# Kernel tuning notes

Hardware: AMD Instinct MI355X
Metric: run time of the kernel (lower is better)

The kernel has to match this reference:

```python
import jax, jax.numpy as jnp
import numpy as np

B, L, D, N, V = 32, 4096, 128, 5, 128  # batch, seq, embed dim, n-gram order, alphabet size


def setup_inputs() -> dict:
    key = jax.random.key(0)
    k1, k2, k3 = jax.random.split(key, 3)
    x = jax.random.randint(k1, (B, L), 0, V, dtype=jnp.int32)
    emb = jax.random.normal(k2, (V, D), dtype=jnp.float32)
    W = jax.random.normal(k3, (V, D * (N - 1)), dtype=jnp.float32) * 0.05
    b = jnp.zeros((V,), dtype=jnp.float32)
    return {"x": x, "emb": emb, "W": W, "b": b}


def reference(x, emb, W, b):
    n1 = N - 1  # context window size
    x_enc = emb[x]  # (B, L, D) embedding gather
    # enc[:, j, k*D:(k+1)*D] = x_enc[:, j - n1 + k] for j >= n1; zeros for j < n1.
    # Build each slot by right-shifting the embedded sequence by (n1 - k).
    Lcur = x.shape[1]
    parts = [jnp.pad(x_enc, ((0, 0), (n1 - k, 0), (0, 0)))[:, :Lcur] for k in range(n1)]
    enc = jnp.concatenate(parts, axis=-1)  # (B, L, n1*D)
    valid = (jnp.arange(Lcur) >= n1)[None, :, None]
    enc = jnp.where(valid, enc, jnp.zeros((), enc.dtype))
    # linear: logits = enc @ W^T + b  -> (B, L, V)
    logits = jnp.einsum("blf,vf->blv", enc, W) + b
    return logits
```

## Files before the change

kernel.cpp:

```cpp
#include <hip/hip_runtime.h>

constexpr int Bn = 32;
constexpr int Ln = 4096;
constexpr int Dn = 128;
constexpr int Vn = 128;
constexpr int N1 = 4;

typedef float vfloat4 __attribute__((ext_vector_type(4)));

__global__ void build_table_kernel(const float* __restrict__ emb,
                                   const float* __restrict__ W,
                                   const float* __restrict__ bias,
                                   float* __restrict__ T) {
    const int kt = blockIdx.x;
    const int k  = kt >> 7;
    const int t  = kt & 127;
    const int v  = threadIdx.x;

    __shared__ float4 e[Dn / 4];
    if (threadIdx.x < Dn / 4) {
        e[threadIdx.x] = ((const float4*)(emb + t * Dn))[threadIdx.x];
    }
    __syncthreads();

    const float4* w = (const float4*)(W + (size_t)v * (Dn * N1) + k * Dn);
    float acc = (k == 0) ? bias[v] : 0.f;
#pragma unroll
    for (int i = 0; i < Dn / 4; ++i) {
        float4 wv = w[i];
        float4 ev = e[i];
        acc += wv.x * ev.x + wv.y * ev.y + wv.z * ev.z + wv.w * ev.w;
    }
    T[(size_t)kt * Vn + v] = acc;
}

__global__ void __launch_bounds__(256)
ngram_logits_kernel(const int* __restrict__ x,
                    const float* __restrict__ T,
                    const float* __restrict__ bias,
                    float* __restrict__ out) {
    const int tid     = blockIdx.x * blockDim.x + threadIdx.x;
    const int vq      = tid & 31;
    const int g       = tid >> 5;
    const int basepos = g << 2;
    const int j0      = basepos & (Ln - 1);

    vfloat4* outq = (vfloat4*)out;

    if (j0 == 0) {
        const vfloat4 bv = ((const vfloat4*)bias)[vq];
#pragma unroll
        for (int i = 0; i < 4; ++i)
            __builtin_nontemporal_store(bv, &outq[(size_t)(basepos + i) * 32 + vq]);
        return;
    }

    const int4 xa = *(const int4*)(x + basepos - 4);
    const int4 xb = *(const int4*)(x + basepos);
    int w[7] = {xa.x, xa.y, xa.z, xa.w, xb.x, xb.y, xb.z};

    const vfloat4* Tq = (const vfloat4*)T;
    vfloat4 acc[4];
#pragma unroll
    for (int i = 0; i < 4; ++i) {
        vfloat4 a = Tq[(size_t)(0 * Vn + w[i + 0]) * 32 + vq];
#pragma unroll
        for (int k = 1; k < N1; ++k) {
            a += Tq[(size_t)(k * Vn + w[i + k]) * 32 + vq];
        }
        acc[i] = a;
    }

#pragma unroll
    for (int i = 0; i < 4; ++i)
        __builtin_nontemporal_store(acc[i], &outq[(size_t)(basepos + i) * 32 + vq]);
}

extern "C" void kernel_launch(void* const* d_in, const int* in_sizes, int n_in,
                              void* d_out, int out_size, void* d_ws, size_t ws_size,
                              hipStream_t stream) {
    const int*   x    = (const int*)d_in[0];
    const float* emb  = (const float*)d_in[1];
    const float* W    = (const float*)d_in[2];
    const float* bias = (const float*)d_in[3];
    float*       out  = (float*)d_out;
    float*       T    = (float*)d_ws;

    build_table_kernel<<<N1 * Vn, Vn, 0, stream>>>(emb, W, bias, T);

    const int total_threads = (Bn * Ln / 4) * (Vn / 4);
    const int block = 256;
    ngram_logits_kernel<<<total_threads / block, block, 0, stream>>>(x, T, bias, out);
}
```

Baseline: 92.77 us.

## Stage vocab-sliced n-gram table in LDS and gather from shared memory

The precomputed table is re-laid out into 8 vocab slices of 16 columns each. Each block copies its 32 KB slice into padded LDS (row stride 20 floats to reduce bank conflicts) and then serves 1024 positions for that slice from LDS rather than from global or L2. Each block covers only 16 output columns, so every output row is written as 64-byte chunks, and the x indices are read once for each of the 8 slices. The launch moves to 1024 blocks of 512 threads.

```diff
diff --git a/kernel.cpp b/kernel.cpp
--- a/kernel.cpp
+++ b/kernel.cpp
@@ -31,49 +31,66 @@
         float4 ev = e[i];
         acc += wv.x * ev.x + wv.y * ev.y + wv.z * ev.z + wv.w * ev.w;
     }
-    T[(size_t)kt * Vn + v] = acc;
+    T[(size_t)(((v >> 4) * N1 + k) * Vn + t) * 16 + (v & 15)] = acc;
 }
 
-__global__ void __launch_bounds__(256)
+constexpr int ROWS    = N1 * Vn;
+constexpr int RSTRIDE = 20;
+
+__global__ void __launch_bounds__(512, 8)
 ngram_logits_kernel(const int* __restrict__ x,
                     const float* __restrict__ T,
                     const float* __restrict__ bias,
                     float* __restrict__ out) {
-    const int tid     = blockIdx.x * blockDim.x + threadIdx.x;
-    const int vq      = tid & 31;
-    const int g       = tid >> 5;
-    const int basepos = g << 2;
-    const int j0      = basepos & (Ln - 1);
+    __shared__ float lds[ROWS * RSTRIDE];
 
-    vfloat4* outq = (vfloat4*)out;
+    const int e  = blockIdx.x & 7;
+    const int pb = blockIdx.x >> 3;
 
-    if (j0 == 0) {
-        const vfloat4 bv = ((const vfloat4*)bias)[vq];
+    {
+        const float4* src = (const float4*)(T + (size_t)e * (ROWS * 16));
+        float4*       dst = (float4*)lds;
 #pragma unroll
-        for (int i = 0; i < 4; ++i)
-            __builtin_nontemporal_store(bv, &outq[(size_t)(basepos + i) * 32 + vq]);
-        return;
+        for (int it = 0; it < 4; ++it) {
+            const int f = it * 512 + threadIdx.x;
+            const int r = f >> 2;
+            const int c = f & 3;
+            dst[r * (RSTRIDE / 4) + c] = src[f];
+        }
     }
+    __syncthreads();
 
-    const int4 xa = *(const int4*)(x + basepos - 4);
-    const int4 xb = *(const int4*)(x + basepos);
-    int w[7] = {xa.x, xa.y, xa.z, xa.w, xb.x, xb.y, xb.z};
-
-    const vfloat4* Tq = (const vfloat4*)T;
-    vfloat4 acc[4];
-#pragma unroll
-    for (int i = 0; i < 4; ++i) {
-        vfloat4 a = Tq[(size_t)(0 * Vn + w[i + 0]) * 32 + vq];
-#pragma unroll
-        for (int k = 1; k < N1; ++k) {
-            a += Tq[(size_t)(k * Vn + w[i + k]) * 32 + vq];
-        }
-        acc[i] = a;
-    }
+    const int vq = threadIdx.x & 3;
+    const int gl = threadIdx.x >> 2;
+    const vfloat4* lv   = (const vfloat4*)lds;
+    vfloat4*       outq = (vfloat4*)out;
 
 #pragma unroll
-    for (int i = 0; i < 4; ++i)
-        __builtin_nontemporal_store(acc[i], &outq[(size_t)(basepos + i) * 32 + vq]);
+    for (int it = 0; it < 2; ++it) {
+        const int basepos = pb * 1024 + it * 512 + gl * 4;
+        vfloat4*  ob      = outq + (size_t)basepos * 32 + e * 4 + vq;
+
+        if ((basepos & (Ln - 1)) == 0) {
+            const vfloat4 bv = ((const vfloat4*)bias)[e * 4 + vq];
+#pragma unroll
+            for (int i = 0; i < 4; ++i)
+                __builtin_nontemporal_store(bv, ob + i * 32);
+            continue;
+        }
+
+        const int4 xa = *(const int4*)(x + basepos - 4);
+        const int4 xb = *(const int4*)(x + basepos);
+        const int  w[7] = {xa.x, xa.y, xa.z, xa.w, xb.x, xb.y, xb.z};
+
+#pragma unroll
+        for (int i = 0; i < 4; ++i) {
+            vfloat4 a = lv[w[i] * 5 + vq];
+#pragma unroll
+            for (int k = 1; k < N1; ++k)
+                a += lv[(k * Vn + w[i + k]) * 5 + vq];
+            __builtin_nontemporal_store(a, ob + i * 32);
+        }
+    }
 }
 
 extern "C" void kernel_launch(void* const* d_in, const int* in_sizes, int n_in,
@@ -88,7 +105,5 @@
 
     build_table_kernel<<<N1 * Vn, Vn, 0, stream>>>(emb, W, bias, T);
 
-    const int total_threads = (Bn * Ln / 4) * (Vn / 4);
-    const int block = 256;
-    ngram_logits_kernel<<<total_threads / block, block, 0, stream>>>(x, T, bias, out);
+    ngram_logits_kernel<<<1024, 512, 0, stream>>>(x, T, bias, out);
 }
```

Result: slower. 100.9 us (+8.8%).
